# Kernel optimization log

Hardware: AMD Instinct MI355X
Metric: run time of the kernel (lower is better)

The kernel has to match this reference:

```python
import jax, jax.numpy as jnp
import numpy as np

B, T, I, H = 1024, 200, 128, 128


def setup_inputs() -> dict:
    key = jax.random.key(0)
    ks = jax.random.split(key, 8)
    s = 1.0 / np.sqrt(I + H)
    return {
        "inputs": jax.random.normal(ks[0], (B, T, I), dtype=jnp.float32),
        "attention_scores": jax.random.uniform(ks[1], (B, T), dtype=jnp.float32),
        "Wz": jax.random.normal(ks[2], (H, I + H), dtype=jnp.float32) * s,
        "bz": jax.random.normal(ks[3], (H,), dtype=jnp.float32) * s,
        "Wr": jax.random.normal(ks[4], (H, I + H), dtype=jnp.float32) * s,
        "br": jax.random.normal(ks[5], (H,), dtype=jnp.float32) * s,
        "Wh": jax.random.normal(ks[6], (H, I + H), dtype=jnp.float32) * s,
        "bh": jax.random.normal(ks[7], (H,), dtype=jnp.float32) * s,
    }


def reference(inputs, attention_scores, Wz, bz, Wr, br, Wh, bh):
    b, t, i = inputs.shape
    h_dim = Wz.shape[0]
    # Split each gate weight into its x-part and h-part:
    # linear(cat(x, h)) == x @ Wx.T + h @ Wh_.T + b
    Wz_x, Wz_h = Wz[:, :i], Wz[:, i:]
    Wr_x, Wr_h = Wr[:, :i], Wr[:, i:]
    Wh_x, Wh_h = Wh[:, :i], Wh[:, i:]

    # Precompute input projections in one batched GEMM each: [T, B, H]
    xz = jnp.einsum('bti,hi->tbh', inputs, Wz_x) + bz
    xr = jnp.einsum('bti,hi->tbh', inputs, Wr_x) + br
    xh = jnp.einsum('bti,hi->tbh', inputs, Wh_x) + bh
    a = attention_scores.T  # [T, B]

    h0 = jnp.zeros((b, h_dim), dtype=inputs.dtype)

    def step(h, xs):
        xz_t, xr_t, xh_t, a_t = xs
        z = jax.nn.sigmoid(xz_t + h @ Wz_h.T)
        r = jax.nn.sigmoid(xr_t + h @ Wr_h.T)
        h_tilde = jnp.tanh(xh_t + (r * h) @ Wh_h.T)
        z_prime = a_t[:, None] * z
        h_new = (1.0 - z_prime) * h + z_prime * h_tilde
        return h_new, None

    h_final, _ = jax.lax.scan(step, h0, (xz, xr, xh, a))
    return h_final
```

## Files before the change

### kernel.cpp

```cpp
#include <hip/hip_runtime.h>


#define T_N   200
#define I_DIM 128
#define H_DIM 128
#define NBLK  64

typedef float  f32x4  __attribute__((ext_vector_type(4)));
typedef __bf16 bf16x4 __attribute__((ext_vector_type(4)));
typedef __bf16 bf16x8 __attribute__((ext_vector_type(8)));

#define GATE_BYTES 4096
#define PB_BYTES   (3 * GATE_BYTES)
#define PRE_BYTES  ((size_t)T_N * NBLK * PB_BYTES)

#define LDA_STRIDE 264
#define LATT_STRIDE 201

__device__ __forceinline__ float fast_sigmoid(float x) {
  float e = __builtin_amdgcn_exp2f(-1.4426950408889634f * x);
  return __builtin_amdgcn_rcpf(1.0f + e);
}
__device__ __forceinline__ float fast_tanh(float x) {
  float e = __builtin_amdgcn_exp2f(2.8853900817779268f * x);
  return 1.0f - 2.0f * __builtin_amdgcn_rcpf(1.0f + e);
}
__device__ __forceinline__ void barrier_lds() {
  asm volatile("s_waitcnt lgkmcnt(0)\n\ts_barrier" ::: "memory");
}
__device__ __forceinline__ bf16x8 pack8(float4 a, float4 b) {
  bf16x8 t;
  t[0] = (__bf16)a.x; t[1] = (__bf16)a.y; t[2] = (__bf16)a.z; t[3] = (__bf16)a.w;
  t[4] = (__bf16)b.x; t[5] = (__bf16)b.y; t[6] = (__bf16)b.z; t[7] = (__bf16)b.w;
  return t;
}
__device__ __forceinline__ int swz(int row, int bytecol) {
  return row * 256 + (bytecol ^ ((row & 7) << 4));
}

#define TCHUNK 10
__global__ __launch_bounds__(256, 2)
void xproj_kernel(const float* __restrict__ inputs,
                  const float* __restrict__ Wz, const float* __restrict__ bz,
                  const float* __restrict__ Wr, const float* __restrict__ br,
                  const float* __restrict__ Wh, const float* __restrict__ bh,
                  char* __restrict__ pre) {
  const int tid  = threadIdx.x;
  const int w    = tid >> 6;
  const int l    = tid & 63;
  const int l15  = l & 15;
  const int lk   = l >> 4;
  const int bblk = blockIdx.x & (NBLK - 1);
  const int t0   = (blockIdx.x >> 6) * TCHUNK;
  const int r0   = bblk * 16;

  bf16x8 wb[24];
  f32x4  bias4[6];
  #pragma unroll
  for (int s = 0; s < 6; ++s) {
    int hid0 = w * 32 + (s & 1) * 16;
    const float* Wp; const float* bp;
    if (s < 2)      { Wp = Wz; bp = bz; }
    else if (s < 4) { Wp = Wr; bp = br; }
    else            { Wp = Wh; bp = bh; }
    float4 bv = *(const float4*)&bp[hid0 + lk * 4];
    bias4[s][0] = bv.x; bias4[s][1] = bv.y; bias4[s][2] = bv.z; bias4[s][3] = bv.w;
    const float* Wrow = Wp + (size_t)(hid0 + l15) * 256;
    #pragma unroll
    for (int kt = 0; kt < 4; ++kt) {
      const float* p = Wrow + kt * 32 + lk * 8;
      wb[s * 4 + kt] = pack8(*(const float4*)p, *(const float4*)(p + 4));
    }
  }

  const float* xbase = inputs + (size_t)(r0 + l15) * (T_N * I_DIM);

  #pragma unroll 2
  for (int ti = 0; ti < TCHUNK; ++ti) {
    const int t = t0 + ti;
    bf16x8 xf[4];
    #pragma unroll
    for (int kt = 0; kt < 4; ++kt) {
      const float* p = xbase + (size_t)t * I_DIM + kt * 32 + lk * 8;
      xf[kt] = pack8(*(const float4*)p, *(const float4*)(p + 4));
    }
    f32x4 acc[6];
    #pragma unroll
    for (int s = 0; s < 6; ++s) acc[s] = bias4[s];
    #pragma unroll
    for (int kt = 0; kt < 4; ++kt)
      #pragma unroll
      for (int s = 0; s < 6; ++s)
        acc[s] = __builtin_amdgcn_mfma_f32_16x16x32_bf16(wb[s * 4 + kt], xf[kt], acc[s], 0, 0, 0);

    char* base = pre + ((size_t)t * NBLK + bblk) * PB_BYTES;
    #pragma unroll
    for (int s = 0; s < 6; ++s) {
      int g      = s >> 1;
      int hidgrp = w * 8 + (s & 1) * 4 + lk;
      bf16x4 v;
      v[0] = (__bf16)acc[s][0]; v[1] = (__bf16)acc[s][1];
      v[2] = (__bf16)acc[s][2]; v[3] = (__bf16)acc[s][3];
      *(bf16x4*)(base + g * GATE_BYTES + hidgrp * 128 + l15 * 8) = v;
    }
  }
}

__global__ __launch_bounds__(512, 1)
void augru_rec_kernel(const char* __restrict__ pre,
                      const float* __restrict__ attn,
                      const float* __restrict__ Wz,
                      const float* __restrict__ Wr,
                      const float* __restrict__ Wh,
                      float* __restrict__ out) {
  __shared__ __align__(16) short lds_h [16 * 128];
  __shared__ __align__(16) short lds_rh[16 * 128];
  __shared__ float lds_att[T_N * 16];

  const int tid   = threadIdx.x;
  const int w     = tid >> 6;
  const int l     = tid & 63;
  const int l15   = l & 15;
  const int lk    = l >> 4;
  const int r0    = blockIdx.x * 16;
  const int myhid = w * 16 + lk * 4;

  for (int idx = tid; idx < T_N * 16; idx += 512) {
    int t = idx >> 4, b = idx & 15;
    lds_att[idx] = attn[(size_t)(r0 + b) * T_N + t];
  }
  for (int idx = tid; idx < 16 * 128; idx += 512) lds_h[idx] = 0;

  bf16x8 wzH[4], wrH[4], whH[4];
  {
    const float* pz = Wz + (size_t)(w * 16 + l15) * 256 + 128;
    const float* pr = Wr + (size_t)(w * 16 + l15) * 256 + 128;
    const float* ph = Wh + (size_t)(w * 16 + l15) * 256 + 128;
    #pragma unroll
    for (int kt = 0; kt < 4; ++kt) {
      const float* a = pz + kt * 32 + lk * 8;
      wzH[kt] = pack8(*(const float4*)a, *(const float4*)(a + 4));
      const float* b = pr + kt * 32 + lk * 8;
      wrH[kt] = pack8(*(const float4*)b, *(const float4*)(b + 4));
      const float* c = ph + kt * 32 + lk * 8;
      whH[kt] = pack8(*(const float4*)c, *(const float4*)(c + 4));
    }
  }

  float hreg[4];
  #pragma unroll
  for (int q = 0; q < 4; ++q) hreg[q] = 0.0f;

  const char* pb = pre + (size_t)blockIdx.x * PB_BYTES + (w * 4 + lk) * 128 + l15 * 8;
  const size_t tstride = (size_t)NBLK * PB_BYTES;
  bf16x4 pf[2][3];
  #pragma unroll
  for (int d = 0; d < 2; ++d)
    #pragma unroll
    for (int g = 0; g < 3; ++g)
      pf[d][g] = *(const bf16x4*)(pb + d * tstride + g * GATE_BYTES);

  const int wr_off = swz(l15, 32 * w + 8 * lk);

  __syncthreads();

  #pragma unroll 2
  for (int t = 0; t < T_N; ++t) {
    float pzv[4], prv[4], phv[4];
    #pragma unroll
    for (int q = 0; q < 4; ++q) {
      pzv[q] = (float)pf[t & 1][0][q];
      prv[q] = (float)pf[t & 1][1][q];
      phv[q] = (float)pf[t & 1][2][q];
    }
    if (t + 2 < T_N) {
      const char* b = pb + (size_t)(t + 2) * tstride;
      #pragma unroll
      for (int g = 0; g < 3; ++g)
        pf[t & 1][g] = *(const bf16x4*)(b + g * GATE_BYTES);
    }

    bf16x8 hb[4];
    #pragma unroll
    for (int kt = 0; kt < 4; ++kt)
      hb[kt] = *(const bf16x8*)((const char*)lds_h + swz(l15, kt * 64 + lk * 16));
    const float av = lds_att[t * 16 + l15];

    f32x4 zA, zB, rA, rB;
    { f32x4 a; a[0]=pzv[0]; a[1]=pzv[1]; a[2]=pzv[2]; a[3]=pzv[3]; zA = a; }
    { f32x4 a; a[0]=prv[0]; a[1]=prv[1]; a[2]=prv[2]; a[3]=prv[3]; rA = a; }
    { f32x4 z; z[0]=0.f; z[1]=0.f; z[2]=0.f; z[3]=0.f; zB = z; rB = z; }
    zA = __builtin_amdgcn_mfma_f32_16x16x32_bf16(wzH[0], hb[0], zA, 0, 0, 0);
    rA = __builtin_amdgcn_mfma_f32_16x16x32_bf16(wrH[0], hb[0], rA, 0, 0, 0);
    zB = __builtin_amdgcn_mfma_f32_16x16x32_bf16(wzH[1], hb[1], zB, 0, 0, 0);
    rB = __builtin_amdgcn_mfma_f32_16x16x32_bf16(wrH[1], hb[1], rB, 0, 0, 0);
    zA = __builtin_amdgcn_mfma_f32_16x16x32_bf16(wzH[2], hb[2], zA, 0, 0, 0);
    rA = __builtin_amdgcn_mfma_f32_16x16x32_bf16(wrH[2], hb[2], rA, 0, 0, 0);
    zB = __builtin_amdgcn_mfma_f32_16x16x32_bf16(wzH[3], hb[3], zB, 0, 0, 0);
    rB = __builtin_amdgcn_mfma_f32_16x16x32_bf16(wrH[3], hb[3], rB, 0, 0, 0);

    bf16x4 rhv;
    #pragma unroll
    for (int q = 0; q < 4; ++q) {
      float rr = fast_sigmoid(rA[q] + rB[q]);
      rhv[q] = (__bf16)(rr * hreg[q]);
    }
    *(bf16x4*)((char*)lds_rh + wr_off) = rhv;
    float zp[4];
    #pragma unroll
    for (int q = 0; q < 4; ++q)
      zp[q] = av * fast_sigmoid(zA[q] + zB[q]);
    barrier_lds();

    bf16x8 rb[4];
    #pragma unroll
    for (int kt = 0; kt < 4; ++kt)
      rb[kt] = *(const bf16x8*)((const char*)lds_rh + swz(l15, kt * 64 + lk * 16));
    f32x4 hA, hB;
    { f32x4 a; a[0]=phv[0]; a[1]=phv[1]; a[2]=phv[2]; a[3]=phv[3]; hA = a; }
    { f32x4 z; z[0]=0.f; z[1]=0.f; z[2]=0.f; z[3]=0.f; hB = z; }
    hA = __builtin_amdgcn_mfma_f32_16x16x32_bf16(whH[0], rb[0], hA, 0, 0, 0);
    hB = __builtin_amdgcn_mfma_f32_16x16x32_bf16(whH[1], rb[1], hB, 0, 0, 0);
    hA = __builtin_amdgcn_mfma_f32_16x16x32_bf16(whH[2], rb[2], hA, 0, 0, 0);
    hB = __builtin_amdgcn_mfma_f32_16x16x32_bf16(whH[3], rb[3], hB, 0, 0, 0);

    bf16x4 hbv;
    #pragma unroll
    for (int q = 0; q < 4; ++q) {
      float ht = fast_tanh(hA[q] + hB[q]);
      float hn = __builtin_fmaf(zp[q], ht - hreg[q], hreg[q]);
      hreg[q] = hn;
      hbv[q] = (__bf16)hn;
    }
    *(bf16x4*)((char*)lds_h + wr_off) = hbv;
    barrier_lds();
  }

  float4 o;
  o.x = hreg[0]; o.y = hreg[1]; o.z = hreg[2]; o.w = hreg[3];
  *(float4*)&out[(size_t)(r0 + l15) * H_DIM + myhid] = o;
}

__global__ __launch_bounds__(256, 1)
void augru_kernel(const float* __restrict__ inputs,
                  const float* __restrict__ attn,
                  const float* __restrict__ Wz, const float* __restrict__ bz,
                  const float* __restrict__ Wr, const float* __restrict__ br,
                  const float* __restrict__ Wh, const float* __restrict__ bh,
                  float* __restrict__ out) {
  __shared__ __align__(16) short lds_a[16 * LDA_STRIDE];
  __shared__ float lds_att[16 * LATT_STRIDE];

  const int tid = threadIdx.x;
  const int w   = tid >> 6;
  const int l   = tid & 63;
  const int l15 = l & 15;
  const int lk  = l >> 4;
  const int r0  = blockIdx.x * 16;

  for (int idx = tid; idx < 16 * T_N; idx += 256) {
    int row = idx / T_N, t = idx - row * T_N;
    lds_att[row * LATT_STRIDE + t] = attn[(size_t)(r0 + row) * T_N + t];
  }
  for (int idx = tid; idx < 16 * H_DIM; idx += 256) {
    int row = idx >> 7, c = idx & 127;
    lds_a[row * LDA_STRIDE + c] = 0;
  }

  bf16x8 w1[32];
  float  bias1[4];
  #pragma unroll
  for (int ct = 0; ct < 4; ++ct) {
    int n = w * 32 + (ct & 1) * 16 + l15;
    const float* Wp; float bv;
    if (ct < 2) { Wp = Wz + (size_t)n * 256; bv = bz[n]; }
    else        { Wp = Wr + (size_t)n * 256; bv = br[n]; }
    bias1[ct] = bv;
    #pragma unroll
    for (int kt = 0; kt < 8; ++kt) {
      const float* p = Wp + kt * 32 + lk * 8;
      w1[ct * 8 + kt] = pack8(*(const float4*)p, *(const float4*)(p + 4));
    }
  }
  bf16x8 w2[16];
  float  bias2[2];
  #pragma unroll
  for (int ct = 0; ct < 2; ++ct) {
    int n = w * 32 + ct * 16 + l15;
    bias2[ct] = bh[n];
    const float* Wp = Wh + (size_t)n * 256;
    #pragma unroll
    for (int kt = 0; kt < 8; ++kt) {
      const float* p = Wp + kt * 32 + lk * 8;
      w2[ct * 8 + kt] = pack8(*(const float4*)p, *(const float4*)(p + 4));
    }
  }

  float hreg[2][4];
  #pragma unroll
  for (int ct = 0; ct < 2; ++ct)
    #pragma unroll
    for (int q = 0; q < 4; ++q) hreg[ct][q] = 0.0f;

  const float* xbase = inputs + (size_t)(r0 + l15) * (T_N * I_DIM);
  bf16x8 xfrag[4];
  #pragma unroll
  for (int kt = 0; kt < 4; ++kt) {
    const float* p = xbase + kt * 32 + lk * 8;
    xfrag[kt] = pack8(*(const float4*)p, *(const float4*)(p + 4));
  }

  __syncthreads();

  float4 xr0[4], xr1[4];
  for (int t = 0; t < T_N; ++t) {
    if (t + 1 < T_N) {
      #pragma unroll
      for (int kt = 0; kt < 4; ++kt) {
        const float* p = xbase + (size_t)(t + 1) * I_DIM + kt * 32 + lk * 8;
        xr0[kt] = *(const float4*)p;
        xr1[kt] = *(const float4*)(p + 4);
      }
    }
    bf16x8 hfrag[4];
    #pragma unroll
    for (int kt = 0; kt < 4; ++kt)
      hfrag[kt] = *(const bf16x8*)&lds_a[l15 * LDA_STRIDE + kt * 32 + lk * 8];
    float av[4];
    #pragma unroll
    for (int q = 0; q < 4; ++q) av[q] = lds_att[(lk * 4 + q) * LATT_STRIDE + t];

    f32x4 acc[4];
    #pragma unroll
    for (int ct = 0; ct < 4; ++ct) {
      f32x4 a; a[0] = bias1[ct]; a[1] = bias1[ct]; a[2] = bias1[ct]; a[3] = bias1[ct];
      acc[ct] = a;
    }
    #pragma unroll
    for (int kt = 0; kt < 4; ++kt)
      #pragma unroll
      for (int ct = 0; ct < 4; ++ct)
        acc[ct] = __builtin_amdgcn_mfma_f32_16x16x32_bf16(xfrag[kt], w1[ct * 8 + kt], acc[ct], 0, 0, 0);

    f32x4 acc2[2];
    #pragma unroll
    for (int ct = 0; ct < 2; ++ct) {
      f32x4 a; a[0] = bias2[ct]; a[1] = bias2[ct]; a[2] = bias2[ct]; a[3] = bias2[ct];
      acc2[ct] = a;
    }
    #pragma unroll
    for (int kt = 0; kt < 4; ++kt)
      #pragma unroll
      for (int ct = 0; ct < 2; ++ct)
        acc2[ct] = __builtin_amdgcn_mfma_f32_16x16x32_bf16(xfrag[kt], w2[ct * 8 + kt], acc2[ct], 0, 0, 0);

    #pragma unroll
    for (int kt = 0; kt < 4; ++kt)
      #pragma unroll
      for (int ct = 0; ct < 4; ++ct)
        acc[ct] = __builtin_amdgcn_mfma_f32_16x16x32_bf16(hfrag[kt], w1[ct * 8 + 4 + kt], acc[ct], 0, 0, 0);

    float zp[2][4];
    #pragma unroll
    for (int ct = 0; ct < 2; ++ct) {
      int col = w * 32 + ct * 16 + l15;
      #pragma unroll
      for (int q = 0; q < 4; ++q) {
        int row = lk * 4 + q;
        zp[ct][q] = av[q] * fast_sigmoid(acc[ct][q]);
        float rr = fast_sigmoid(acc[2 + ct][q]);
        __bf16 rhb = (__bf16)(rr * hreg[ct][q]);
        lds_a[row * LDA_STRIDE + 128 + col] = __builtin_bit_cast(short, rhb);
      }
    }
    barrier_lds();

    bf16x8 rfrag[4];
    #pragma unroll
    for (int kt = 0; kt < 4; ++kt)
      rfrag[kt] = *(const bf16x8*)&lds_a[l15 * LDA_STRIDE + 128 + kt * 32 + lk * 8];
    #pragma unroll
    for (int kt = 0; kt < 4; ++kt)
      #pragma unroll
      for (int ct = 0; ct < 2; ++ct)
        acc2[ct] = __builtin_amdgcn_mfma_f32_16x16x32_bf16(rfrag[kt], w2[ct * 8 + 4 + kt], acc2[ct], 0, 0, 0);

    if (t + 1 < T_N) {
      #pragma unroll
      for (int kt = 0; kt < 4; ++kt)
        xfrag[kt] = pack8(xr0[kt], xr1[kt]);
    }

    #pragma unroll
    for (int ct = 0; ct < 2; ++ct) {
      int col = w * 32 + ct * 16 + l15;
      #pragma unroll
      for (int q = 0; q < 4; ++q) {
        int row = lk * 4 + q;
        float ht = fast_tanh(acc2[ct][q]);
        float ho = hreg[ct][q];
        float hn = __builtin_fmaf(zp[ct][q], ht - ho, ho);
        hreg[ct][q] = hn;
        __bf16 hb = (__bf16)hn;
        lds_a[row * LDA_STRIDE + col] = __builtin_bit_cast(short, hb);
      }
    }
    barrier_lds();
  }

  #pragma unroll
  for (int ct = 0; ct < 2; ++ct) {
    int col = w * 32 + ct * 16 + l15;
    #pragma unroll
    for (int q = 0; q < 4; ++q) {
      int row = lk * 4 + q;
      out[(size_t)(r0 + row) * H_DIM + col] = hreg[ct][q];
    }
  }
}

extern "C" void kernel_launch(void* const* d_in, const int* in_sizes, int n_in,
                              void* d_out, int out_size, void* d_ws, size_t ws_size,
                              hipStream_t stream) {
  (void)in_sizes; (void)n_in; (void)out_size;
  const float* inputs = (const float*)d_in[0];
  const float* attn   = (const float*)d_in[1];
  const float* Wz     = (const float*)d_in[2];
  const float* bz     = (const float*)d_in[3];
  const float* Wr     = (const float*)d_in[4];
  const float* br     = (const float*)d_in[5];
  const float* Wh     = (const float*)d_in[6];
  const float* bh     = (const float*)d_in[7];
  float* out = (float*)d_out;

  if (ws_size >= PRE_BYTES) {
    char* pre = (char*)d_ws;
    xproj_kernel<<<NBLK * (T_N / TCHUNK), 256, 0, stream>>>(inputs, Wz, bz, Wr, br, Wh, bh, pre);
    augru_rec_kernel<<<NBLK, 512, 0, stream>>>(pre, attn, Wz, Wr, Wh, out);
  } else {
    augru_kernel<<<NBLK, 256, 0, stream>>>(inputs, attn, Wz, bz, Wr, br, Wh, bh, out);
  }
}
```

Before: 276.0 us.

## Fuse input projection and recurrence into one pipelined kernel with flags

Merges the input-projection kernel and the recurrent kernel into a single launch. The first 64 blocks run the recurrence, and 640 producer blocks compute the projections in 20-step time chunks. Each producer publishes a per-chunk flag with release semantics, and the recurrent blocks spin on those flags before prefetching each chunk. This overlaps the projection GEMM with the sequential recurrence and removes the kernel boundary, at the cost of a memset launch, spin-waits, and a large static LDS allocation that limits occupancy for the producer blocks. It relies on the recurrent blocks being scheduled so they do not starve the producers.

```diff
diff --git a/kernel.cpp b/kernel.cpp
--- a/kernel.cpp
+++ b/kernel.cpp
@@ -5,6 +5,9 @@
 #define I_DIM 128
 #define H_DIM 128
 #define NBLK  64
+#define CHUNK_T  20
+#define NCHUNK   10
+#define XBLK     (NBLK * NCHUNK)
 
 typedef float  f32x4  __attribute__((ext_vector_type(4)));
 typedef __bf16 bf16x4 __attribute__((ext_vector_type(4)));
@@ -13,6 +16,7 @@
 #define GATE_BYTES 4096
 #define PB_BYTES   (3 * GATE_BYTES)
 #define PRE_BYTES  ((size_t)T_N * NBLK * PB_BYTES)
+#define FLAG_BYTES 4096
 
 #define LDA_STRIDE 264
 #define LATT_STRIDE 201
@@ -37,91 +41,100 @@
 __device__ __forceinline__ int swz(int row, int bytecol) {
   return row * 256 + (bytecol ^ ((row & 7) << 4));
 }
-
-#define TCHUNK 10
-__global__ __launch_bounds__(256, 2)
-void xproj_kernel(const float* __restrict__ inputs,
-                  const float* __restrict__ Wz, const float* __restrict__ bz,
-                  const float* __restrict__ Wr, const float* __restrict__ br,
-                  const float* __restrict__ Wh, const float* __restrict__ bh,
-                  char* __restrict__ pre) {
-  const int tid  = threadIdx.x;
-  const int w    = tid >> 6;
-  const int l    = tid & 63;
-  const int l15  = l & 15;
-  const int lk   = l >> 4;
-  const int bblk = blockIdx.x & (NBLK - 1);
-  const int t0   = (blockIdx.x >> 6) * TCHUNK;
-  const int r0   = bblk * 16;
-
-  bf16x8 wb[24];
-  f32x4  bias4[6];
-  #pragma unroll
-  for (int s = 0; s < 6; ++s) {
-    int hid0 = w * 32 + (s & 1) * 16;
-    const float* Wp; const float* bp;
-    if (s < 2)      { Wp = Wz; bp = bz; }
-    else if (s < 4) { Wp = Wr; bp = br; }
-    else            { Wp = Wh; bp = bh; }
-    float4 bv = *(const float4*)&bp[hid0 + lk * 4];
-    bias4[s][0] = bv.x; bias4[s][1] = bv.y; bias4[s][2] = bv.z; bias4[s][3] = bv.w;
-    const float* Wrow = Wp + (size_t)(hid0 + l15) * 256;
-    #pragma unroll
-    for (int kt = 0; kt < 4; ++kt) {
-      const float* p = Wrow + kt * 32 + lk * 8;
-      wb[s * 4 + kt] = pack8(*(const float4*)p, *(const float4*)(p + 4));
-    }
-  }
-
-  const float* xbase = inputs + (size_t)(r0 + l15) * (T_N * I_DIM);
-
-  #pragma unroll 2
-  for (int ti = 0; ti < TCHUNK; ++ti) {
-    const int t = t0 + ti;
-    bf16x8 xf[4];
-    #pragma unroll
-    for (int kt = 0; kt < 4; ++kt) {
-      const float* p = xbase + (size_t)t * I_DIM + kt * 32 + lk * 8;
-      xf[kt] = pack8(*(const float4*)p, *(const float4*)(p + 4));
-    }
-    f32x4 acc[6];
-    #pragma unroll
-    for (int s = 0; s < 6; ++s) acc[s] = bias4[s];
-    #pragma unroll
-    for (int kt = 0; kt < 4; ++kt)
-      #pragma unroll
-      for (int s = 0; s < 6; ++s)
-        acc[s] = __builtin_amdgcn_mfma_f32_16x16x32_bf16(wb[s * 4 + kt], xf[kt], acc[s], 0, 0, 0);
-
-    char* base = pre + ((size_t)t * NBLK + bblk) * PB_BYTES;
+__device__ __forceinline__ void wait_flag(const int* f) {
+  while (__hip_atomic_load(f, __ATOMIC_ACQUIRE, __HIP_MEMORY_SCOPE_AGENT) == 0) {
+    __builtin_amdgcn_s_sleep(2);
+  }
+}
+
+__global__ __launch_bounds__(512, 1)
+void augru_pipe_kernel(const float* __restrict__ inputs,
+                       const float* __restrict__ attn,
+                       const float* __restrict__ Wz, const float* __restrict__ bz,
+                       const float* __restrict__ Wr, const float* __restrict__ br,
+                       const float* __restrict__ Wh, const float* __restrict__ bh,
+                       float* __restrict__ out,
+                       char* __restrict__ pre, int* __restrict__ flags) {
+  __shared__ __align__(16) char lds_all[86016];
+
+  const int tid = threadIdx.x;
+  const int l   = tid & 63;
+  const int l15 = l & 15;
+  const int lk  = l >> 4;
+
+  if (blockIdx.x >= NBLK) {
+    const int bidp = blockIdx.x - NBLK;
+    const int bblk = bidp & (NBLK - 1);
+    const int c    = bidp >> 6;
+    const int w8   = tid >> 6;
+    const int half = w8 >> 2;
+    const int w    = w8 & 3;
+    const int t0   = c * CHUNK_T + half * (CHUNK_T / 2);
+    const int r0   = bblk * 16;
+
+    bf16x8 wb[24];
+    f32x4  bias4[6];
     #pragma unroll
     for (int s = 0; s < 6; ++s) {
-      int g      = s >> 1;
-      int hidgrp = w * 8 + (s & 1) * 4 + lk;
-      bf16x4 v;
-      v[0] = (__bf16)acc[s][0]; v[1] = (__bf16)acc[s][1];
-      v[2] = (__bf16)acc[s][2]; v[3] = (__bf16)acc[s][3];
-      *(bf16x4*)(base + g * GATE_BYTES + hidgrp * 128 + l15 * 8) = v;
-    }
-  }
-}
-
-__global__ __launch_bounds__(512, 1)
-void augru_rec_kernel(const char* __restrict__ pre,
-                      const float* __restrict__ attn,
-                      const float* __restrict__ Wz,
-                      const float* __restrict__ Wr,
-                      const float* __restrict__ Wh,
-                      float* __restrict__ out) {
-  __shared__ __align__(16) short lds_h [16 * 128];
-  __shared__ __align__(16) short lds_rh[16 * 128];
-  __shared__ float lds_att[T_N * 16];
-
-  const int tid   = threadIdx.x;
+      int hid0 = w * 32 + (s & 1) * 16;
+      const float* Wp; const float* bp;
+      if (s < 2)      { Wp = Wz; bp = bz; }
+      else if (s < 4) { Wp = Wr; bp = br; }
+      else            { Wp = Wh; bp = bh; }
+      float4 bv = *(const float4*)&bp[hid0 + lk * 4];
+      bias4[s][0] = bv.x; bias4[s][1] = bv.y; bias4[s][2] = bv.z; bias4[s][3] = bv.w;
+      const float* Wrow = Wp + (size_t)(hid0 + l15) * 256;
+      #pragma unroll
+      for (int kt = 0; kt < 4; ++kt) {
+        const float* p = Wrow + kt * 32 + lk * 8;
+        wb[s * 4 + kt] = pack8(*(const float4*)p, *(const float4*)(p + 4));
+      }
+    }
+
+    const float* xbase = inputs + (size_t)(r0 + l15) * (T_N * I_DIM);
+
+    #pragma unroll 2
+    for (int ti = 0; ti < CHUNK_T / 2; ++ti) {
+      const int t = t0 + ti;
+      bf16x8 xf[4];
+      #pragma unroll
+      for (int kt = 0; kt < 4; ++kt) {
+        const float* p = xbase + (size_t)t * I_DIM + kt * 32 + lk * 8;
+        xf[kt] = pack8(*(const float4*)p, *(const float4*)(p + 4));
+      }
+      f32x4 acc[6];
+      #pragma unroll
+      for (int s = 0; s < 6; ++s) acc[s] = bias4[s];
+      #pragma unroll
+      for (int kt = 0; kt < 4; ++kt)
+        #pragma unroll
+        for (int s = 0; s < 6; ++s)
+          acc[s] = __builtin_amdgcn_mfma_f32_16x16x32_bf16(wb[s * 4 + kt], xf[kt], acc[s], 0, 0, 0);
+
+      char* base = pre + ((size_t)t * NBLK + bblk) * PB_BYTES;
+      #pragma unroll
+      for (int s = 0; s < 6; ++s) {
+        int g      = s >> 1;
+        int hidgrp = w * 8 + (s & 1) * 4 + lk;
+        bf16x4 v;
+        v[0] = (__bf16)acc[s][0]; v[1] = (__bf16)acc[s][1];
+        v[2] = (__bf16)acc[s][2]; v[3] = (__bf16)acc[s][3];
+        *(bf16x4*)(base + g * GATE_BYTES + hidgrp * 128 + l15 * 8) = v;
+      }
+    }
+
+    __syncthreads();
+    __threadfence();
+    if (tid == 0)
+      __hip_atomic_store(&flags[c * NBLK + bblk], 1, __ATOMIC_RELEASE, __HIP_MEMORY_SCOPE_AGENT);
+    return;
+  }
+
+  short* lds_h  = (short*)lds_all;
+  short* lds_rh = (short*)(lds_all + 4096);
+  float* lds_att = (float*)(lds_all + 8192);
+
   const int w     = tid >> 6;
-  const int l     = tid & 63;
-  const int l15   = l & 15;
-  const int lk    = l >> 4;
   const int r0    = blockIdx.x * 16;
   const int myhid = w * 16 + lk * 4;
 
@@ -142,8 +155,8 @@
       wzH[kt] = pack8(*(const float4*)a, *(const float4*)(a + 4));
       const float* b = pr + kt * 32 + lk * 8;
       wrH[kt] = pack8(*(const float4*)b, *(const float4*)(b + 4));
-      const float* c = ph + kt * 32 + lk * 8;
-      whH[kt] = pack8(*(const float4*)c, *(const float4*)(c + 4));
+      const float* cc = ph + kt * 32 + lk * 8;
+      whH[kt] = pack8(*(const float4*)cc, *(const float4*)(cc + 4));
     }
   }
 
@@ -153,6 +166,9 @@
 
   const char* pb = pre + (size_t)blockIdx.x * PB_BYTES + (w * 4 + lk) * 128 + l15 * 8;
   const size_t tstride = (size_t)NBLK * PB_BYTES;
+
+  wait_flag(&flags[0 * NBLK + blockIdx.x]);
+
   bf16x4 pf[2][3];
   #pragma unroll
   for (int d = 0; d < 2; ++d)
@@ -174,6 +190,8 @@
       phv[q] = (float)pf[t & 1][2][q];
     }
     if (t + 2 < T_N) {
+      if (((t + 2) % CHUNK_T) == 0)
+        wait_flag(&flags[((t + 2) / CHUNK_T) * NBLK + blockIdx.x]);
       const char* b = pb + (size_t)(t + 2) * tstride;
       #pragma unroll
       for (int g = 0; g < 3; ++g)
@@ -433,10 +451,12 @@
   const float* bh     = (const float*)d_in[7];
   float* out = (float*)d_out;
 
-  if (ws_size >= PRE_BYTES) {
-    char* pre = (char*)d_ws;
-    xproj_kernel<<<NBLK * (T_N / TCHUNK), 256, 0, stream>>>(inputs, Wz, bz, Wr, br, Wh, bh, pre);
-    augru_rec_kernel<<<NBLK, 512, 0, stream>>>(pre, attn, Wz, Wr, Wh, out);
+  if (ws_size >= PRE_BYTES + FLAG_BYTES) {
+    char* pre   = (char*)d_ws;
+    int*  flags = (int*)(pre + PRE_BYTES);
+    hipMemsetAsync(flags, 0, NCHUNK * NBLK * sizeof(int), stream);
+    augru_pipe_kernel<<<NBLK + XBLK, 512, 0, stream>>>(
+        inputs, attn, Wz, bz, Wr, br, Wh, bh, out, pre, flags);
   } else {
     augru_kernel<<<NBLK, 256, 0, stream>>>(inputs, attn, Wz, bz, Wr, br, Wh, bh, out);
   }
```

After: 390.2 us. 1.41x slower.

## Stage x tiles through double-buffered LDS and enlarge xproj time chunk

Applied to the files above, without the earlier changes.

In the input-projection kernel, each timestep's 16x128 x tile is now loaded once per block with coalesced loads, converted to bf16 and written into a swizzled double-buffered LDS area. Before, each of the four waves loaded the same tile from global memory on its own. The next step's tile is prefetched into registers while the MFMAs run. TCHUNK goes from 10 to 25, so fewer blocks each reuse their weight registers over more timesteps, at the cost of one barrier per step and less parallelism.

```diff
diff --git a/kernel.cpp b/kernel.cpp
--- a/kernel.cpp
+++ b/kernel.cpp
@@ -5,6 +5,7 @@
 #define I_DIM 128
 #define H_DIM 128
 #define NBLK  64
+#define TCHUNK 25
 
 typedef float  f32x4  __attribute__((ext_vector_type(4)));
 typedef __bf16 bf16x4 __attribute__((ext_vector_type(4)));
@@ -38,13 +39,14 @@
   return row * 256 + (bytecol ^ ((row & 7) << 4));
 }
 
-#define TCHUNK 10
 __global__ __launch_bounds__(256, 2)
 void xproj_kernel(const float* __restrict__ inputs,
                   const float* __restrict__ Wz, const float* __restrict__ bz,
                   const float* __restrict__ Wr, const float* __restrict__ br,
                   const float* __restrict__ Wh, const float* __restrict__ bh,
                   char* __restrict__ pre) {
+  __shared__ __align__(16) char lds_x[2 * 4096];
+
   const int tid  = threadIdx.x;
   const int w    = tid >> 6;
   const int l    = tid & 63;
@@ -53,6 +55,11 @@
   const int bblk = blockIdx.x & (NBLK - 1);
   const int t0   = (blockIdx.x >> 6) * TCHUNK;
   const int r0   = bblk * 16;
+
+  const int crow  = tid >> 4;
+  const int cslot = tid & 15;
+  const float* xsrc = inputs + (size_t)(r0 + crow) * (T_N * I_DIM) + cslot * 8;
+  const int cwoff = swz(crow, cslot * 16);
 
   bf16x8 wb[24];
   f32x4  bias4[6];
@@ -73,17 +80,30 @@
     }
   }
 
-  const float* xbase = inputs + (size_t)(r0 + l15) * (T_N * I_DIM);
+  {
+    const float* p = xsrc + (size_t)t0 * I_DIM;
+    float4 a = *(const float4*)p;
+    float4 b = *(const float4*)(p + 4);
+    *(bf16x8*)(lds_x + cwoff) = pack8(a, b);
+  }
+  barrier_lds();
 
   #pragma unroll 2
   for (int ti = 0; ti < TCHUNK; ++ti) {
     const int t = t0 + ti;
+    float4 ra, rb2;
+    if (ti + 1 < TCHUNK) {
+      const float* p = xsrc + (size_t)(t + 1) * I_DIM;
+      ra  = *(const float4*)p;
+      rb2 = *(const float4*)(p + 4);
+    }
+
+    char* bufc = lds_x + ((ti & 1) ? 4096 : 0);
     bf16x8 xf[4];
     #pragma unroll
-    for (int kt = 0; kt < 4; ++kt) {
-      const float* p = xbase + (size_t)t * I_DIM + kt * 32 + lk * 8;
-      xf[kt] = pack8(*(const float4*)p, *(const float4*)(p + 4));
-    }
+    for (int kt = 0; kt < 4; ++kt)
+      xf[kt] = *(const bf16x8*)(bufc + swz(l15, kt * 64 + lk * 16));
+
     f32x4 acc[6];
     #pragma unroll
     for (int s = 0; s < 6; ++s) acc[s] = bias4[s];
@@ -103,6 +123,12 @@
       v[2] = (__bf16)acc[s][2]; v[3] = (__bf16)acc[s][3];
       *(bf16x4*)(base + g * GATE_BYTES + hidgrp * 128 + l15 * 8) = v;
     }
+
+    if (ti + 1 < TCHUNK) {
+      char* bufn = lds_x + (((ti + 1) & 1) ? 4096 : 0);
+      *(bf16x8*)(bufn + cwoff) = pack8(ra, rb2);
+    }
+    barrier_lds();
   }
 }
 
@@ -142,8 +168,8 @@
       wzH[kt] = pack8(*(const float4*)a, *(const float4*)(a + 4));
       const float* b = pr + kt * 32 + lk * 8;
       wrH[kt] = pack8(*(const float4*)b, *(const float4*)(b + 4));
-      const float* c = ph + kt * 32 + lk * 8;
-      whH[kt] = pack8(*(const float4*)c, *(const float4*)(c + 4));
+      const float* cc = ph + kt * 32 + lk * 8;
+      whH[kt] = pack8(*(const float4*)cc, *(const float4*)(cc + 4));
     }
   }
 
```

Result: faster. 236.0 us (-14.5%).
